# Performance work log

Measured on AMD Instinct MI355X. Metric: run time of the kernel, lower is better.

The kernel has to match this reference:

```python
import jax, jax.numpy as jnp
import numpy as np

N_EXPERTS = 8
TOP_K = 2


def setup_inputs() -> dict:
    key = jax.random.key(0)
    ks = jax.random.split(key, 5)
    B, S, D = 4, 2048, 1024
    H = 2 * D  # SwiGLU hidden = 2 * embeddings_dims
    E = N_EXPERTS
    scale_d = 1.0 / np.sqrt(D)
    scale_h = 1.0 / np.sqrt(H)
    return {
        "x": jax.random.normal(ks[0], (B, S, D), dtype=jnp.float32),
        "Wg": jax.random.normal(ks[1], (D, E), dtype=jnp.float32) * scale_d,
        "W1": jax.random.normal(ks[2], (E, D, H), dtype=jnp.float32) * scale_d,
        "W2": jax.random.normal(ks[3], (E, D, H), dtype=jnp.float32) * scale_d,
        "W3": jax.random.normal(ks[4], (E, H, D), dtype=jnp.float32) * scale_h,
    }


def _swiglu(x, w1, w2, w3):
    # x: [B,S,D]; w1,w2: [D,H]; w3: [H,D]
    a = x @ w1
    swish = a * jax.nn.sigmoid(a)
    return (swish * (x @ w2)) @ w3


def reference(x, Wg, W1, W2, W3):
    # Gating (noisy_topk disabled -> deterministic path)
    gate = x @ Wg                                   # [B,S,E]
    top_vals, top_idx = jax.lax.top_k(gate, TOP_K)  # [B,S,K]
    probs = jax.nn.softmax(top_vals, axis=-1)       # softmax over top-k values

    out = jnp.zeros_like(x)
    for e in range(N_EXPERTS):
        # combine weight for expert e per token (0 if not routed)
        w_e = jnp.sum(jnp.where(top_idx == e, probs, 0.0), axis=-1)  # [B,S]
        out = out + _swiglu(x, W1[e], W2[e], W3[e]) * w_e[..., None]
    return out
```

## Files before the change

kernel.cpp:

```cpp
#include <hip/hip_runtime.h>
#include <stdint.h>
#include <math.h>

#define NTOK  8192
#define DIM   1024
#define HID   2048
#define NE    8

typedef __attribute__((ext_vector_type(8))) short short8;
typedef __attribute__((ext_vector_type(4))) float f32x4;

__device__ __forceinline__ unsigned short f2bf(float f) {
  union { float f; unsigned u; } a; a.f = f;
  unsigned u = a.u;
  u += 0x7fffu + ((u >> 16) & 1u);
  return (unsigned short)(u >> 16);
}

__device__ __forceinline__ void gl2lds16(const unsigned short* g, unsigned short* l) {
  __builtin_amdgcn_global_load_lds(
      (const __attribute__((address_space(1))) unsigned int*)g,
      (__attribute__((address_space(3))) unsigned int*)l,
      16, 0, 0);
}

__global__ __launch_bounds__(256) void transpose_cast_kernel(
    const float* __restrict__ in, unsigned short* __restrict__ out, int R, int C) {
  __shared__ unsigned short tileT[64][72];
  int e = blockIdx.z;
  const float* ine = in + (size_t)e * R * C + (size_t)(blockIdx.y * 64) * C + blockIdx.x * 64;
  unsigned short* oute = out + (size_t)e * R * C + (size_t)(blockIdx.x * 64) * R + blockIdx.y * 64;
  int t = threadIdx.x;
  #pragma unroll
  for (int i = 0; i < 4; i++) {
    int idx = t + i * 256;
    int r = idx >> 4, c = (idx & 15) * 4;
    float4 v = *(const float4*)(ine + (size_t)r * C + c);
    tileT[c + 0][r] = f2bf(v.x);
    tileT[c + 1][r] = f2bf(v.y);
    tileT[c + 2][r] = f2bf(v.z);
    tileT[c + 3][r] = f2bf(v.w);
  }
  __syncthreads();
  #pragma unroll
  for (int i = 0; i < 2; i++) {
    int idx = t + i * 256;
    int rr = idx >> 3, cc = (idx & 7) * 8;
    *(uint4*)(oute + (size_t)rr * R + cc) = *(const uint4*)(&tileT[rr][cc]);
  }
}

__global__ __launch_bounds__(256) void gate_kernel(
    const float* __restrict__ x, const float* __restrict__ Wg,
    unsigned short* __restrict__ xb,
    int* __restrict__ eidx, float* __restrict__ eprob, int* __restrict__ cnt) {
  if (blockIdx.x == 0 && threadIdx.x < NE) cnt[threadIdx.x] = 0;
  int wid = threadIdx.x >> 6;
  int lane = threadIdx.x & 63;
  int t = blockIdx.x * 4 + wid;
  const float* xr = x + (size_t)t * DIM;
  unsigned short* xbr = xb + (size_t)t * DIM;
  float acc[NE];
  #pragma unroll
  for (int e = 0; e < NE; e++) acc[e] = 0.f;
  #pragma unroll
  for (int it = 0; it < DIM / 64; it++) {
    int d = it * 64 + lane;
    float xv = xr[d];
    xbr[d] = f2bf(xv);
    const float4* wr = (const float4*)(Wg + d * NE);
    float4 w0 = wr[0], w1 = wr[1];
    acc[0] += xv * w0.x; acc[1] += xv * w0.y; acc[2] += xv * w0.z; acc[3] += xv * w0.w;
    acc[4] += xv * w1.x; acc[5] += xv * w1.y; acc[6] += xv * w1.z; acc[7] += xv * w1.w;
  }
  #pragma unroll
  for (int e = 0; e < NE; e++) {
    float v = acc[e];
    #pragma unroll
    for (int off = 32; off > 0; off >>= 1) v += __shfl_xor(v, off);
    acc[e] = v;
  }
  if (lane == 0) {
    int i0 = 0; float v0 = acc[0];
    #pragma unroll
    for (int e = 1; e < NE; e++) if (acc[e] > v0) { v0 = acc[e]; i0 = e; }
    int i1 = -1; float v1 = -3.4e38f;
    #pragma unroll
    for (int e = 0; e < NE; e++) if (e != i0 && acc[e] > v1) { v1 = acc[e]; i1 = e; }
    float e1 = expf(v1 - v0);
    float p0 = 1.f / (1.f + e1);
    float p1 = e1 / (1.f + e1);
    eidx[t] = i0 | (i1 << 16);
    eprob[2 * t] = p0;
    eprob[2 * t + 1] = p1;
  }
}

__global__ __launch_bounds__(512) void route_kernel(
    const int* __restrict__ eidx,
    int* __restrict__ cnt, int* __restrict__ tok_list, int* __restrict__ slotpos) {
  __shared__ int lhist[NE];
  __shared__ int gbase[NE];
  int tid = threadIdx.x;
  if (tid < NE) lhist[tid] = 0;
  __syncthreads();
  int t = blockIdx.x * 512 + tid;
  int pk = eidx[t];
  int i0 = pk & 0xffff, i1 = pk >> 16;
  int l0 = atomicAdd(&lhist[i0], 1);
  int l1 = atomicAdd(&lhist[i1], 1);
  __syncthreads();
  if (tid < NE) gbase[tid] = atomicAdd(&cnt[tid], lhist[tid]);
  __syncthreads();
  int s0 = gbase[i0] + l0;
  int s1 = gbase[i1] + l1;
  tok_list[i0 * NTOK + s0] = t;
  tok_list[i1 * NTOK + s1] = t;
  slotpos[2 * t] = (i0 << 16) | s0;
  slotpos[2 * t + 1] = (i1 << 16) | s1;
}

__global__ __launch_bounds__(256, 3) void gemm1_kernel(
    const unsigned short* __restrict__ xb,
    const unsigned short* __restrict__ w1t,
    const unsigned short* __restrict__ w2t,
    const int* __restrict__ cnt,
    const int* __restrict__ tok_list,
    unsigned short* __restrict__ hbuf) {
  int e = blockIdx.z;
  int count = cnt[e];
  int mt = blockIdx.y;
  if (mt * 128 >= count) return;
  int nt = blockIdx.x;

  __shared__ __align__(16) unsigned short As[128 * 64];
  __shared__ __align__(16) unsigned short Bs1[64 * 64];
  __shared__ __align__(16) unsigned short Bs2[64 * 64];
  __shared__ int toks[128];

  int tid = threadIdx.x;
  if (tid < 128) {
    int r = mt * 128 + tid;
    toks[tid] = tok_list[e * NTOK + (r < count ? r : 0)];
  }
  __syncthreads();

  int wid = tid >> 6, lane = tid & 63;
  int wm = wid >> 1, wn = wid & 1;
  int m16 = lane & 15, quad = lane >> 4;

  const unsigned short* W1e = w1t + (size_t)e * HID * DIM + (size_t)(nt * 64) * DIM;
  const unsigned short* W2e = w2t + (size_t)e * HID * DIM + (size_t)(nt * 64) * DIM;

  const unsigned short* aptr[4];
  #pragma unroll
  for (int i = 0; i < 4; i++) {
    int slot = wid * 256 + i * 64 + lane;
    int r = slot >> 3, c = slot & 7, g = c ^ (r & 7);
    aptr[i] = xb + (size_t)toks[r] * DIM + g * 8;
  }
  const unsigned short *b1p[2], *b2p[2];
  #pragma unroll
  for (int i = 0; i < 2; i++) {
    int slot = wid * 128 + i * 64 + lane;
    int r = slot >> 3, c = slot & 7, g = c ^ (r & 7);
    b1p[i] = W1e + (size_t)r * DIM + g * 8;
    b2p[i] = W2e + (size_t)r * DIM + g * 8;
  }

  f32x4 acc1[4][2], acc2[4][2];
  f32x4 zz = {0.f, 0.f, 0.f, 0.f};
  #pragma unroll
  for (int i = 0; i < 4; i++)
    #pragma unroll
    for (int j = 0; j < 2; j++) { acc1[i][j] = zz; acc2[i][j] = zz; }

  for (int k0 = 0; k0 < DIM; k0 += 64) {
    #pragma unroll
    for (int i = 0; i < 4; i++)
      gl2lds16(aptr[i] + k0, As + (wid * 256 + i * 64) * 8);
    #pragma unroll
    for (int i = 0; i < 2; i++) {
      gl2lds16(b1p[i] + k0, Bs1 + (wid * 128 + i * 64) * 8);
      gl2lds16(b2p[i] + k0, Bs2 + (wid * 128 + i * 64) * 8);
    }
    __syncthreads();
    #pragma unroll
    for (int ks = 0; ks < 2; ks++) {
      int ga = ks * 4 + quad;
      short8 af[4], b1f[2], b2f[2];
      #pragma unroll
      for (int fm = 0; fm < 4; fm++) {
        int ra = wm * 64 + fm * 16 + m16;
        af[fm] = *(const short8*)(As + ra * 64 + (ga ^ (ra & 7)) * 8);
      }
      #pragma unroll
      for (int fn = 0; fn < 2; fn++) {
        int rb = wn * 32 + fn * 16 + m16;
        b1f[fn] = *(const short8*)(Bs1 + rb * 64 + (ga ^ (rb & 7)) * 8);
        b2f[fn] = *(const short8*)(Bs2 + rb * 64 + (ga ^ (rb & 7)) * 8);
      }
      #pragma unroll
      for (int fm = 0; fm < 4; fm++)
        #pragma unroll
        for (int fn = 0; fn < 2; fn++) {
          acc1[fm][fn] = __builtin_amdgcn_mfma_f32_16x16x32_bf16(af[fm], b1f[fn], acc1[fm][fn], 0, 0, 0);
          acc2[fm][fn] = __builtin_amdgcn_mfma_f32_16x16x32_bf16(af[fm], b2f[fn], acc2[fm][fn], 0, 0, 0);
        }
    }
    __syncthreads();
  }

  int hb = 0;
  #pragma unroll
  for (int j = 0; j < NE; j++) if (j < e) hb += cnt[j];
  #pragma unroll
  for (int fm = 0; fm < 4; fm++)
    #pragma unroll
    for (int fn = 0; fn < 2; fn++)
      #pragma unroll
      for (int r = 0; r < 4; r++) {
        int row = wm * 64 + fm * 16 + quad * 4 + r;
        if (mt * 128 + row < count) {
          float a = acc1[fm][fn][r];
          float v = acc2[fm][fn][r];
          float h = (a / (1.f + __expf(-a))) * v;
          int col = nt * 64 + wn * 32 + fn * 16 + m16;
          hbuf[(size_t)(hb + mt * 128 + row) * HID + col] = f2bf(h);
        }
      }
}

__global__ __launch_bounds__(256, 3) void gemm2_kernel(
    const unsigned short* __restrict__ hbuf,
    const unsigned short* __restrict__ w3t,
    const int* __restrict__ cnt,
    float* __restrict__ ybuf) {
  int e = blockIdx.z;
  int count = cnt[e];
  int mt = blockIdx.y;
  if (mt * 128 >= count) return;
  int nt = blockIdx.x;
  int hb = 0;
  #pragma unroll
  for (int j = 0; j < NE; j++) if (j < e) hb += cnt[j];

  __shared__ __align__(16) unsigned short As[128 * 64];
  __shared__ __align__(16) unsigned short Bs[128 * 64];

  int tid = threadIdx.x;
  int wid = tid >> 6, lane = tid & 63;
  int wm = wid >> 1, wn = wid & 1;
  int m16 = lane & 15, quad = lane >> 4;

  const unsigned short* W3e = w3t + (size_t)e * DIM * HID + (size_t)(nt * 128) * HID;

  const unsigned short *aptr[4], *bptr[4];
  #pragma unroll
  for (int i = 0; i < 4; i++) {
    int slot = wid * 256 + i * 64 + lane;
    int r = slot >> 3, c = slot & 7, g = c ^ (r & 7);
    int gr = mt * 128 + r;
    int rc = (gr < count) ? gr : (count - 1);
    aptr[i] = hbuf + (size_t)(hb + rc) * HID + g * 8;
    bptr[i] = W3e + (size_t)r * HID + g * 8;
  }

  f32x4 acc[4][4];
  f32x4 zz = {0.f, 0.f, 0.f, 0.f};
  #pragma unroll
  for (int i = 0; i < 4; i++)
    #pragma unroll
    for (int j = 0; j < 4; j++) acc[i][j] = zz;

  for (int k0 = 0; k0 < HID; k0 += 64) {
    #pragma unroll
    for (int i = 0; i < 4; i++) {
      gl2lds16(aptr[i] + k0, As + (wid * 256 + i * 64) * 8);
      gl2lds16(bptr[i] + k0, Bs + (wid * 256 + i * 64) * 8);
    }
    __syncthreads();
    #pragma unroll
    for (int ks = 0; ks < 2; ks++) {
      int ga = ks * 4 + quad;
      short8 af[4], bf[4];
      #pragma unroll
      for (int fm = 0; fm < 4; fm++) {
        int ra = wm * 64 + fm * 16 + m16;
        af[fm] = *(const short8*)(As + ra * 64 + (ga ^ (ra & 7)) * 8);
      }
      #pragma unroll
      for (int fn = 0; fn < 4; fn++) {
        int rb = wn * 64 + fn * 16 + m16;
        bf[fn] = *(const short8*)(Bs + rb * 64 + (ga ^ (rb & 7)) * 8);
      }
      #pragma unroll
      for (int fm = 0; fm < 4; fm++)
        #pragma unroll
        for (int fn = 0; fn < 4; fn++)
          acc[fm][fn] = __builtin_amdgcn_mfma_f32_16x16x32_bf16(af[fm], bf[fn], acc[fm][fn], 0, 0, 0);
    }
    __syncthreads();
  }

  #pragma unroll
  for (int fm = 0; fm < 4; fm++)
    #pragma unroll
    for (int fn = 0; fn < 4; fn++)
      #pragma unroll
      for (int r = 0; r < 4; r++) {
        int row = wm * 64 + fm * 16 + quad * 4 + r;
        if (mt * 128 + row < count) {
          int col = nt * 128 + wn * 64 + fn * 16 + m16;
          ybuf[(size_t)(hb + mt * 128 + row) * DIM + col] = acc[fm][fn][r];
        }
      }
}

__global__ __launch_bounds__(256) void combine_kernel(
    const float* __restrict__ ybuf, const int* __restrict__ cnt,
    const int* __restrict__ slotpos, const float* __restrict__ eprob,
    float* __restrict__ out) {
  __shared__ int sbase[NE];
  if (threadIdx.x == 0) {
    int s = 0;
    #pragma unroll
    for (int e = 0; e < NE; e++) { sbase[e] = s; s += cnt[e]; }
  }
  __syncthreads();
  int t = blockIdx.x;
  int ps0 = slotpos[2 * t], ps1 = slotpos[2 * t + 1];
  int r0 = sbase[ps0 >> 16] + (ps0 & 0xffff);
  int r1 = sbase[ps1 >> 16] + (ps1 & 0xffff);
  float p0 = eprob[2 * t], p1 = eprob[2 * t + 1];
  int d = threadIdx.x * 4;
  float4 y0 = *(const float4*)(ybuf + (size_t)r0 * DIM + d);
  float4 y1 = *(const float4*)(ybuf + (size_t)r1 * DIM + d);
  float4 o;
  o.x = p0 * y0.x + p1 * y1.x;
  o.y = p0 * y0.y + p1 * y1.y;
  o.z = p0 * y0.z + p1 * y1.z;
  o.w = p0 * y0.w + p1 * y1.w;
  *(float4*)(out + (size_t)t * DIM + d) = o;
}

extern "C" void kernel_launch(void* const* d_in, const int* in_sizes, int n_in,
                              void* d_out, int out_size, void* d_ws, size_t ws_size,
                              hipStream_t stream) {
  const float* x  = (const float*)d_in[0];
  const float* Wg = (const float*)d_in[1];
  const float* W1 = (const float*)d_in[2];
  const float* W2 = (const float*)d_in[3];
  const float* W3 = (const float*)d_in[4];
  float* out = (float*)d_out;

  char* ws = (char*)d_ws;
  size_t off = 0;
  int* cnt = (int*)(ws + off); off += 256;
  int* eidx = (int*)(ws + off); off += (size_t)NTOK * 4;
  float* eprob = (float*)(ws + off); off += (size_t)NTOK * 2 * 4;
  int* slotpos = (int*)(ws + off); off += (size_t)NTOK * 2 * 4;
  int* tok_list = (int*)(ws + off); off += (size_t)NE * NTOK * 4;
  unsigned short* xb  = (unsigned short*)(ws + off); off += (size_t)NTOK * DIM * 2;
  unsigned short* w1t = (unsigned short*)(ws + off); off += (size_t)NE * DIM * HID * 2;
  unsigned short* w2t = (unsigned short*)(ws + off); off += (size_t)NE * DIM * HID * 2;
  unsigned short* w3t = (unsigned short*)(ws + off); off += (size_t)NE * DIM * HID * 2;
  unsigned short* hbuf = (unsigned short*)(ws + off); off += (size_t)NTOK * 2 * HID * 2;
  float* ybuf = (float*)w1t;

  gate_kernel<<<NTOK / 4, 256, 0, stream>>>(x, Wg, xb, eidx, eprob, cnt);
  transpose_cast_kernel<<<dim3(HID / 64, DIM / 64, NE), 256, 0, stream>>>(W1, w1t, DIM, HID);
  transpose_cast_kernel<<<dim3(HID / 64, DIM / 64, NE), 256, 0, stream>>>(W2, w2t, DIM, HID);
  transpose_cast_kernel<<<dim3(DIM / 64, HID / 64, NE), 256, 0, stream>>>(W3, w3t, HID, DIM);
  route_kernel<<<NTOK / 512, 512, 0, stream>>>(eidx, cnt, tok_list, slotpos);
  gemm1_kernel<<<dim3(HID / 64, NTOK / 128, NE), 256, 0, stream>>>(xb, w1t, w2t, cnt, tok_list, hbuf);
  gemm2_kernel<<<dim3(DIM / 128, NTOK / 128, NE), 256, 0, stream>>>(hbuf, w3t, cnt, ybuf);
  combine_kernel<<<NTOK, 256, 0, stream>>>(ybuf, cnt, slotpos, eprob, out);
}
```

Baseline: 527.2 us.

## Merge weight transposes, shrink gemm2 M-tile, store expert outputs as bf16

```diff
diff --git a/kernel.cpp b/kernel.cpp
--- a/kernel.cpp
+++ b/kernel.cpp
@@ -17,6 +17,11 @@
   return (unsigned short)(u >> 16);
 }
 
+__device__ __forceinline__ float bf2f(unsigned short s) {
+  union { unsigned u; float f; } a; a.u = ((unsigned)s) << 16;
+  return a.f;
+}
+
 __device__ __forceinline__ void gl2lds16(const unsigned short* g, unsigned short* l) {
   __builtin_amdgcn_global_load_lds(
       (const __attribute__((address_space(1))) unsigned int*)g,
@@ -24,12 +29,29 @@
       16, 0, 0);
 }
 
-__global__ __launch_bounds__(256) void transpose_cast_kernel(
-    const float* __restrict__ in, unsigned short* __restrict__ out, int R, int C) {
+__global__ __launch_bounds__(256) void transpose_all_kernel(
+    const float* __restrict__ W1, const float* __restrict__ W2, const float* __restrict__ W3,
+    unsigned short* __restrict__ w1t, unsigned short* __restrict__ w2t,
+    unsigned short* __restrict__ w3t) {
   __shared__ unsigned short tileT[64][72];
-  int e = blockIdx.z;
-  const float* ine = in + (size_t)e * R * C + (size_t)(blockIdx.y * 64) * C + blockIdx.x * 64;
-  unsigned short* oute = out + (size_t)e * R * C + (size_t)(blockIdx.x * 64) * R + blockIdx.y * 64;
+  int b = blockIdx.x;
+  int which = b >> 12;
+  int rem = b & 4095;
+  const float* in;
+  unsigned short* out;
+  int R, C, bx, by, e;
+  if (which < 2) {
+    R = DIM; C = HID;
+    bx = rem & 31; by = (rem >> 5) & 15; e = rem >> 9;
+    in = (which == 0 ? W1 : W2);
+    out = (which == 0 ? w1t : w2t);
+  } else {
+    R = HID; C = DIM;
+    bx = rem & 15; by = (rem >> 4) & 31; e = rem >> 9;
+    in = W3; out = w3t;
+  }
+  const float* ine = in + (size_t)e * R * C + (size_t)(by * 64) * C + bx * 64;
+  unsigned short* oute = out + (size_t)e * R * C + (size_t)(bx * 64) * R + by * 64;
   int t = threadIdx.x;
   #pragma unroll
   for (int i = 0; i < 4; i++) {
@@ -231,73 +253,78 @@
       }
 }
 
-__global__ __launch_bounds__(256, 3) void gemm2_kernel(
+__global__ __launch_bounds__(256, 4) void gemm2_kernel(
     const unsigned short* __restrict__ hbuf,
     const unsigned short* __restrict__ w3t,
     const int* __restrict__ cnt,
-    float* __restrict__ ybuf) {
+    unsigned short* __restrict__ ybuf) {
   int e = blockIdx.z;
   int count = cnt[e];
   int mt = blockIdx.y;
-  if (mt * 128 >= count) return;
+  if (mt * 64 >= count) return;
   int nt = blockIdx.x;
   int hb = 0;
   #pragma unroll
   for (int j = 0; j < NE; j++) if (j < e) hb += cnt[j];
 
-  __shared__ __align__(16) unsigned short As[128 * 64];
+  __shared__ __align__(16) unsigned short As[64 * 64];
   __shared__ __align__(16) unsigned short Bs[128 * 64];
 
   int tid = threadIdx.x;
   int wid = tid >> 6, lane = tid & 63;
-  int wm = wid >> 1, wn = wid & 1;
   int m16 = lane & 15, quad = lane >> 4;
 
   const unsigned short* W3e = w3t + (size_t)e * DIM * HID + (size_t)(nt * 128) * HID;
 
-  const unsigned short *aptr[4], *bptr[4];
-  #pragma unroll
-  for (int i = 0; i < 4; i++) {
-    int slot = wid * 256 + i * 64 + lane;
+  const unsigned short *aptr[2], *bptr[4];
+  #pragma unroll
+  for (int i = 0; i < 2; i++) {
+    int slot = tid + 256 * i;
     int r = slot >> 3, c = slot & 7, g = c ^ (r & 7);
-    int gr = mt * 128 + r;
+    int gr = mt * 64 + r;
     int rc = (gr < count) ? gr : (count - 1);
     aptr[i] = hbuf + (size_t)(hb + rc) * HID + g * 8;
+  }
+  #pragma unroll
+  for (int i = 0; i < 4; i++) {
+    int slot = tid + 256 * i;
+    int r = slot >> 3, c = slot & 7, g = c ^ (r & 7);
     bptr[i] = W3e + (size_t)r * HID + g * 8;
   }
 
-  f32x4 acc[4][4];
+  f32x4 acc[4][2];
   f32x4 zz = {0.f, 0.f, 0.f, 0.f};
   #pragma unroll
   for (int i = 0; i < 4; i++)
     #pragma unroll
-    for (int j = 0; j < 4; j++) acc[i][j] = zz;
+    for (int j = 0; j < 2; j++) acc[i][j] = zz;
 
   for (int k0 = 0; k0 < HID; k0 += 64) {
     #pragma unroll
-    for (int i = 0; i < 4; i++) {
-      gl2lds16(aptr[i] + k0, As + (wid * 256 + i * 64) * 8);
-      gl2lds16(bptr[i] + k0, Bs + (wid * 256 + i * 64) * 8);
-    }
+    for (int i = 0; i < 2; i++)
+      gl2lds16(aptr[i] + k0, As + (tid >> 6) * 0 + ((size_t)(256 * i) + (tid & ~63) + (tid & 63)) * 8);
+    #pragma unroll
+    for (int i = 0; i < 4; i++)
+      gl2lds16(bptr[i] + k0, Bs + ((size_t)(256 * i) + tid) * 8);
     __syncthreads();
     #pragma unroll
     for (int ks = 0; ks < 2; ks++) {
       int ga = ks * 4 + quad;
-      short8 af[4], bf[4];
+      short8 af[4], bf[2];
       #pragma unroll
       for (int fm = 0; fm < 4; fm++) {
-        int ra = wm * 64 + fm * 16 + m16;
+        int ra = fm * 16 + m16;
         af[fm] = *(const short8*)(As + ra * 64 + (ga ^ (ra & 7)) * 8);
       }
       #pragma unroll
-      for (int fn = 0; fn < 4; fn++) {
-        int rb = wn * 64 + fn * 16 + m16;
+      for (int fn = 0; fn < 2; fn++) {
+        int rb = wid * 32 + fn * 16 + m16;
         bf[fn] = *(const short8*)(Bs + rb * 64 + (ga ^ (rb & 7)) * 8);
       }
       #pragma unroll
       for (int fm = 0; fm < 4; fm++)
         #pragma unroll
-        for (int fn = 0; fn < 4; fn++)
+        for (int fn = 0; fn < 2; fn++)
           acc[fm][fn] = __builtin_amdgcn_mfma_f32_16x16x32_bf16(af[fm], bf[fn], acc[fm][fn], 0, 0, 0);
     }
     __syncthreads();
@@ -306,19 +333,19 @@
   #pragma unroll
   for (int fm = 0; fm < 4; fm++)
     #pragma unroll
-    for (int fn = 0; fn < 4; fn++)
+    for (int fn = 0; fn < 2; fn++)
       #pragma unroll
       for (int r = 0; r < 4; r++) {
-        int row = wm * 64 + fm * 16 + quad * 4 + r;
-        if (mt * 128 + row < count) {
-          int col = nt * 128 + wn * 64 + fn * 16 + m16;
-          ybuf[(size_t)(hb + mt * 128 + row) * DIM + col] = acc[fm][fn][r];
+        int row = fm * 16 + quad * 4 + r;
+        if (mt * 64 + row < count) {
+          int col = nt * 128 + wid * 32 + fn * 16 + m16;
+          ybuf[(size_t)(hb + mt * 64 + row) * DIM + col] = f2bf(acc[fm][fn][r]);
         }
       }
 }
 
 __global__ __launch_bounds__(256) void combine_kernel(
-    const float* __restrict__ ybuf, const int* __restrict__ cnt,
+    const unsigned short* __restrict__ ybuf, const int* __restrict__ cnt,
     const int* __restrict__ slotpos, const float* __restrict__ eprob,
     float* __restrict__ out) {
   __shared__ int sbase[NE];
@@ -328,20 +355,23 @@
     for (int e = 0; e < NE; e++) { sbase[e] = s; s += cnt[e]; }
   }
   __syncthreads();
-  int t = blockIdx.x;
-  int ps0 = slotpos[2 * t], ps1 = slotpos[2 * t + 1];
-  int r0 = sbase[ps0 >> 16] + (ps0 & 0xffff);
-  int r1 = sbase[ps1 >> 16] + (ps1 & 0xffff);
-  float p0 = eprob[2 * t], p1 = eprob[2 * t + 1];
   int d = threadIdx.x * 4;
-  float4 y0 = *(const float4*)(ybuf + (size_t)r0 * DIM + d);
-  float4 y1 = *(const float4*)(ybuf + (size_t)r1 * DIM + d);
-  float4 o;
-  o.x = p0 * y0.x + p1 * y1.x;
-  o.y = p0 * y0.y + p1 * y1.y;
-  o.z = p0 * y0.z + p1 * y1.z;
-  o.w = p0 * y0.w + p1 * y1.w;
-  *(float4*)(out + (size_t)t * DIM + d) = o;
+  #pragma unroll
+  for (int i = 0; i < 8; i++) {
+    int t = blockIdx.x * 8 + i;
+    int ps0 = slotpos[2 * t], ps1 = slotpos[2 * t + 1];
+    int r0 = sbase[ps0 >> 16] + (ps0 & 0xffff);
+    int r1 = sbase[ps1 >> 16] + (ps1 & 0xffff);
+    float p0 = eprob[2 * t], p1 = eprob[2 * t + 1];
+    ushort4 y0 = *(const ushort4*)(ybuf + (size_t)r0 * DIM + d);
+    ushort4 y1 = *(const ushort4*)(ybuf + (size_t)r1 * DIM + d);
+    float4 o;
+    o.x = p0 * bf2f(y0.x) + p1 * bf2f(y1.x);
+    o.y = p0 * bf2f(y0.y) + p1 * bf2f(y1.y);
+    o.z = p0 * bf2f(y0.z) + p1 * bf2f(y1.z);
+    o.w = p0 * bf2f(y0.w) + p1 * bf2f(y1.w);
+    *(float4*)(out + (size_t)t * DIM + d) = o;
+  }
 }
 
 extern "C" void kernel_launch(void* const* d_in, const int* in_sizes, int n_in,
@@ -366,14 +396,12 @@
   unsigned short* w2t = (unsigned short*)(ws + off); off += (size_t)NE * DIM * HID * 2;
   unsigned short* w3t = (unsigned short*)(ws + off); off += (size_t)NE * DIM * HID * 2;
   unsigned short* hbuf = (unsigned short*)(ws + off); off += (size_t)NTOK * 2 * HID * 2;
-  float* ybuf = (float*)w1t;
+  unsigned short* ybuf = w1t;
 
   gate_kernel<<<NTOK / 4, 256, 0, stream>>>(x, Wg, xb, eidx, eprob, cnt);
-  transpose_cast_kernel<<<dim3(HID / 64, DIM / 64, NE), 256, 0, stream>>>(W1, w1t, DIM, HID);
-  transpose_cast_kernel<<<dim3(HID / 64, DIM / 64, NE), 256, 0, stream>>>(W2, w2t, DIM, HID);
-  transpose_cast_kernel<<<dim3(DIM / 64, HID / 64, NE), 256, 0, stream>>>(W3, w3t, HID, DIM);
+  transpose_all_kernel<<<3 * 4096, 256, 0, stream>>>(W1, W2, W3, w1t, w2t, w3t);
   route_kernel<<<NTOK / 512, 512, 0, stream>>>(eidx, cnt, tok_list, slotpos);
   gemm1_kernel<<<dim3(HID / 64, NTOK / 128, NE), 256, 0, stream>>>(xb, w1t, w2t, cnt, tok_list, hbuf);
-  gemm2_kernel<<<dim3(DIM / 128, NTOK / 128, NE), 256, 0, stream>>>(hbuf, w3t, cnt, ybuf);
-  combine_kernel<<<NTOK, 256, 0, stream>>>(ybuf, cnt, slotpos, eprob, out);
-}
+  gemm2_kernel<<<dim3(DIM / 128, NTOK / 64, NE), 256, 0, stream>>>(hbuf, w3t, cnt, ybuf);
+  combine_kernel<<<NTOK / 8, 256, 0, stream>>>(ybuf, cnt, slotpos, eprob, out);
+}
```

Result: faster. 515.0 us (-2.3%).
